# Kernel tuning notes

Hardware: AMD Instinct MI355X
Metric: run time of the kernel (lower is better)

The kernel has to match this reference:

```python
import jax, jax.numpy as jnp
import numpy as np

D_STATE = 16
LOW_RANK = 6


def _scan_fwd(t):
    # 'interwave' scan: (B, stream, signal, C, H, W) -> (stream, B, C, H*W*signal)
    st, B, C = t.shape[1], t.shape[0], t.shape[3]
    t = jnp.transpose(t, (1, 0, 3, 4, 5, 2))  # stream,B,C,H,W,signal
    return t.reshape(st, B, C, -1)


def _scan_bwd(t, sg, H, W):
    # inverse 'interwave': (stream, B, C, H*W*sg) -> (B, stream, sg, C, H, W)
    st, B, C, _ = t.shape
    t = t.reshape(st, B, C, H, W, sg)
    return jnp.transpose(t, (1, 0, 5, 2, 3, 4))


def _layernorm(t, w, b):
    # LayerNorm over last (channel) axis, eps=1e-5 (torch default)
    mu = t.mean(-1, keepdims=True)
    var = t.var(-1, keepdims=True)
    return (t - mu) * jax.lax.rsqrt(var + 1e-5) * w + b


def reference(x, x_proj_weight, dt_projs_weight, dt_projs_bias, A_logs, Ds, norm_weight, norm_bias):
    B, S, C, H, W = x.shape
    stream = S + 1
    G = 4 * stream            # scan_direction * stream groups
    N = D_STATE
    R = LOW_RANK
    L = S * H * W             # unistream_length
    i = jnp.arange(S - 1)
    j = jnp.arange(S)

    # ---- CommDiffSS2DScan (cross-scan) ----
    x_comm_0 = _scan_fwd(x[:, None])                                  # (1,B,C,L)
    x_comm_1 = _scan_fwd(jnp.swapaxes(x, -1, -2)[:, None])
    x_dif = x[:, :, None] - x[:, None, :]                             # (B,S,S,C,H,W)
    x_dif = x_dif.at[:, i, i].set(x_dif[:, i, S - 1])
    x_dif = x_dif.at[:, :, S - 1].set(x)
    x_diff_0 = _scan_fwd(x_dif)                                       # (S,B,C,L)
    x_diff_1 = _scan_fwd(jnp.swapaxes(x_dif, -1, -2))
    xs0 = jnp.concatenate([x_diff_0, x_comm_0], 0)                    # (stream,B,C,L)
    xs1 = jnp.concatenate([x_diff_1, x_comm_1], 0)
    xs = jnp.stack([xs0, xs1, xs0[..., ::-1], xs1[..., ::-1]], 0)     # (4,stream,B,C,L)
    xs = jnp.transpose(xs, (2, 0, 1, 3, 4))                           # (B,4,stream,C,L)

    # ---- input-dependent projections ----
    x_dbl = jnp.einsum('bkscl,kspc->bkspl', xs, x_proj_weight)        # (B,4,stream,R+2N,L)
    dts, Bs, Cs = jnp.split(x_dbl, [R, R + N], axis=3)
    dts = jnp.einsum('bksrl,kscr->bkscl', dts, dt_projs_weight)       # (B,4,stream,C,L)

    u = xs.reshape(B, G, C, L)
    delta = jax.nn.softplus(dts.reshape(B, G, C, L) + dt_projs_bias.reshape(G, C)[None, :, :, None])
    A = -jnp.exp(A_logs).reshape(G, C, N)
    Bm = Bs.reshape(B, G, N, L)
    Cm = Cs.reshape(B, G, N, L)

    # ---- selective scan along L ----
    def step(h, inp):
        u_, d_, b_, c_ = inp                                          # (B,G,C),(B,G,C),(B,G,N),(B,G,N)
        h = h * jnp.exp(d_[..., None] * A) + (d_ * u_)[..., None] * b_[:, :, None, :]
        return h, jnp.einsum('bgcn,bgn->bgc', h, c_)

    h0 = jnp.zeros((B, G, C, N), x.dtype)
    _, ys = jax.lax.scan(step, h0, (jnp.moveaxis(u, -1, 0), jnp.moveaxis(delta, -1, 0),
                                    jnp.moveaxis(Bm, -1, 0), jnp.moveaxis(Cm, -1, 0)))
    ys = jnp.moveaxis(ys, 0, -1) + Ds.reshape(G, C)[None, :, :, None] * u  # (B,G,C,L)

    # ---- CommDiffSS2DMerge (cross-merge) ----
    ys = jnp.transpose(ys.reshape(B, 4, stream, C, L), (1, 2, 0, 3, 4))   # (4,stream,B,C,L)
    ys = ys[:2] + ys[2:, ..., ::-1]                                       # (2,stream,B,C,L)
    yd = _scan_bwd(ys[0, :S], S, H, W) + jnp.swapaxes(_scan_bwd(ys[1, :S], S, W, H), -1, -2)
    y = yd[:, :, S - 1]
    yd = yd.at[:, i, S - 1].set(yd[:, i, i])
    yd = yd.at[:, j, j].set(0.0)
    y_dif_extend = yd.sum(2)
    y_com = (_scan_bwd(ys[0, S:], S, H, W) + jnp.swapaxes(_scan_bwd(ys[1, S:], S, W, H), -1, -2)).reshape(B, S, C, H, W)

    tocl = lambda t: jnp.transpose(t, (0, 1, 3, 4, 2))  # channels-last for out_norm
    return (_layernorm(tocl(y), norm_weight, norm_bias),
            _layernorm(tocl(y_com), norm_weight, norm_bias),
            _layernorm(tocl(y_dif_extend), norm_weight, norm_bias))


def setup_inputs() -> dict:
    key = jax.random.key(0)
    ks = jax.random.split(key, 6)
    B, S, C, H, W = 4, 2, 96, 32, 32
    stream = S + 1
    G = 4 * stream
    N, R = D_STATE, LOW_RANK
    P = N + N + R
    return {
        'x': jax.random.normal(ks[0], (B, S, C, H, W), jnp.float32),
        'x_proj_weight': jax.random.normal(ks[1], (4, stream, P, C), jnp.float32) * 0.1,
        'dt_projs_weight': jax.random.normal(ks[2], (4, stream, C, R), jnp.float32) * 0.1,
        'dt_projs_bias': jax.random.uniform(ks[3], (G * C,), jnp.float32) * 0.1,
        'A_logs': jax.random.uniform(ks[4], (G * C, N), jnp.float32),
        'Ds': jax.random.normal(ks[5], (G * C,), jnp.float32) * 0.1,
        'norm_weight': jnp.ones((C,), jnp.float32),
        'norm_bias': jnp.zeros((C,), jnp.float32),
    }
```

## Files before the change

kernel.cpp:

```cpp
#include <hip/hip_runtime.h>
#include <math.h>

typedef float f4 __attribute__((ext_vector_type(4)));
typedef float f2 __attribute__((ext_vector_type(2)));

#define L_LEN 2048
#define C_DIM 96
#define N_DIM 16
#define R_DIM 6
#define G_DIM 12
#define B_DIM 4
#define NCHUNK 64
#define CLEN 32
#define BGC (B_DIM * G_DIM * C_DIM)
#define VS 136

#define SZ_DELTA (B_DIM * G_DIM * L_LEN * C_DIM)
#define SZ_BC (B_DIM * G_DIM * N_DIM * L_LEN)
#define SZ_U6 (B_DIM * 6 * C_DIM * L_LEN)
#define SZ_Y (B_DIM * G_DIM * C_DIM * L_LEN)
#define SZ_H (BGC * NCHUNK * N_DIM)
#define SZ_S (BGC * NCHUNK)
#define SZ_X (B_DIM * 2 * C_DIM * 1024)
#define SZ_WPAD (G_DIM * 40 * C_DIM)

__device__ __forceinline__ float fexp2(float x) { return __builtin_amdgcn_exp2f(x); }
__device__ __forceinline__ f2 pkfma(f2 a, f2 b, f2 c) { return __builtin_elementwise_fma(a, b, c); }

__device__ __forceinline__ float softplus_f(float x)
{
    float sp = __logf(1.f + __expf(x));
    return (x > 20.f) ? x : sp;
}

__global__ __launch_bounds__(256) void k0_xT(
    const float* __restrict__ x, float* __restrict__ xT)
{
    __shared__ float t[32][33];
    int img = blockIdx.x;
    const float* src = x + (size_t)img * 1024;
    float* dst = xT + (size_t)img * 1024;
    int tx = threadIdx.x & 31, ty = threadIdx.x >> 5;
#pragma unroll
    for (int r = 0; r < 32; r += 8) t[ty + r][tx] = src[(ty + r) * 32 + tx];
    __syncthreads();
#pragma unroll
    for (int r = 0; r < 32; r += 8) dst[(ty + r) * 32 + tx] = t[tx][ty + r];
}

__global__ __launch_bounds__(256) void k0b_padw(
    const float* __restrict__ xpw, float* __restrict__ wpad)
{
    int i = blockIdx.x * 256 + (int)threadIdx.x;
    if (i >= G_DIM * 40 * C_DIM) return;
    int g = i / (40 * C_DIM);
    int rem = i - g * 40 * C_DIM;
    int p = rem / C_DIM, c = rem - (rem / C_DIM) * C_DIM;
    wpad[i] = (p < 38) ? xpw[((size_t)g * 38 + p) * C_DIM + c] : 0.f;
}

__global__ __launch_bounds__(256) void k1_proj(
    const float* __restrict__ x, const float* __restrict__ xT,
    const float* __restrict__ wpad, const float* __restrict__ dtw,
    const float* __restrict__ dtb,
    float* __restrict__ deltaT, float* __restrict__ Bsw,
    float* __restrict__ Csw, float* __restrict__ u6T)
{
    __shared__ char smem[C_DIM * VS * 4];
    float* Vsh = (float*)smem;
    float (*Psh)[132] = (float(*)[132])smem;

    int blk = blockIdx.x;
    int ltile = blk & 15;
    int bks = blk >> 4;
    int g = bks % G_DIM;
    int b = bks / G_DIM;
    const bool rev = (g >= 6);
    int gu = rev ? (g - 6) : g;
    int k = gu / 3, s = gu % 3;
    int l0 = ltile * 128;
    int bg = b * G_DIM + g;
    int tid = (int)threadIdx.x;

    const float* xb = (k ? xT : x) + (size_t)b * 2 * C_DIM * 1024;

#pragma unroll
    for (int j = 0; j < 12; ++j) {
        int e = tid + j * 256;
        int c = e >> 5;
        int llq = (e & 31) * 4;
        int pp = rev ? (1022 - ((l0 + llq) >> 1)) : ((l0 + llq) >> 1);
        f2 x0 = *(const f2*)(xb + (size_t)c * 1024 + pp);
        f2 x1 = *(const f2*)(xb + (size_t)(C_DIM + c) * 1024 + pp);
        f4 v;
        if (!rev) {
            if (s == 2)      { v[0] = x0.x; v[1] = x1.x; v[2] = x0.y; v[3] = x1.y; }
            else if (s == 1) { v[0] = x1.x - x0.x; v[1] = x1.x; v[2] = x1.y - x0.y; v[3] = x1.y; }
            else             { v[0] = x0.x - x1.x; v[1] = x0.x; v[2] = x0.y - x1.y; v[3] = x0.y; }
        } else {
            if (s == 2)      { v[0] = x1.y; v[1] = x0.y; v[2] = x1.x; v[3] = x0.x; }
            else if (s == 1) { v[0] = x1.y; v[1] = x1.y - x0.y; v[2] = x1.x; v[3] = x1.x - x0.x; }
            else             { v[0] = x0.y; v[1] = x0.y - x1.y; v[2] = x0.x; v[3] = x0.x - x1.x; }
        }
        *(f4*)(Vsh + c * VS + llq) = v;
    }
    __syncthreads();

    if (!rev) {
        size_t ub = ((size_t)(b * 6 + g) * L_LEN + l0) * C_DIM;
#pragma unroll
        for (int j = 0; j < 12; ++j) {
            int e = tid + j * 256;
            int lidx = e / 24;
            int c4 = (e - lidx * 24) * 4;
            f4 v = { Vsh[(c4 + 0) * VS + lidx], Vsh[(c4 + 1) * VS + lidx],
                     Vsh[(c4 + 2) * VS + lidx], Vsh[(c4 + 3) * VS + lidx] };
            *(f4*)(u6T + ub + (size_t)lidx * C_DIM + c4) = v;
        }
    }

    int ll = tid & 63;
    int P0 = __builtin_amdgcn_readfirstlane((tid >> 6) * 10);
    const float* wp = wpad + (size_t)g * 3840 + (size_t)P0 * C_DIM;

    f2 acc2[10];
#pragma unroll
    for (int p = 0; p < 10; ++p) acc2[p] = (f2){0.f, 0.f};

    for (int cb = 0; cb < C_DIM; cb += 8) {
        f2 vc2[8];
#pragma unroll
        for (int i = 0; i < 8; ++i)
            vc2[i] = *(const f2*)(Vsh + (cb + i) * VS + 2 * ll);
#pragma unroll
        for (int p = 0; p < 10; ++p) {
#pragma unroll
            for (int q = 0; q < 2; ++q) {
                f4 w = *(const f4*)(wp + p * C_DIM + cb + q * 4);
#pragma unroll
                for (int i = 0; i < 4; ++i)
                    acc2[p] = pkfma((f2){w[i], w[i]}, vc2[q * 4 + i], acc2[p]);
            }
        }
    }

    __syncthreads();
#pragma unroll
    for (int p = 0; p < 10; ++p) {
        Psh[P0 + p][2 * ll] = acc2[p].x;
        Psh[P0 + p][2 * ll + 1] = acc2[p].y;
    }
    __syncthreads();
#pragma unroll
    for (int half = 0; half < 2; ++half) {
        int q = tid & 3, lx = (tid >> 2) + half * 64;
        f4 bv = { Psh[6 + q * 4 + 0][lx], Psh[6 + q * 4 + 1][lx],
                  Psh[6 + q * 4 + 2][lx], Psh[6 + q * 4 + 3][lx] };
        *(f4*)(Bsw + ((size_t)bg * L_LEN + l0 + lx) * N_DIM + q * 4) = bv;
        f4 cv = { Psh[22 + q * 4 + 0][lx], Psh[22 + q * 4 + 1][lx],
                  Psh[22 + q * 4 + 2][lx], Psh[22 + q * 4 + 3][lx] };
        *(f4*)(Csw + ((size_t)bg * L_LEN + l0 + lx) * N_DIM + q * 4) = cv;
    }
    const float* wdg = dtw + (size_t)g * C_DIM * R_DIM;
    const float* biasg = dtb + g * C_DIM;
    size_t db = ((size_t)bg * L_LEN + l0) * C_DIM;
#pragma unroll
    for (int it = 0; it < 24; ++it) {
        int e = tid + it * 256;
        int lp = e / 96, c = e - (e / 96) * 96;
        const float* wrow = wdg + c * R_DIM;
        f2 ds2 = { biasg[c], biasg[c] };
#pragma unroll
        for (int r = 0; r < R_DIM; ++r) {
            f2 pv = { Psh[r][2 * lp], Psh[r][2 * lp + 1] };
            ds2 = pkfma((f2){wrow[r], wrow[r]}, pv, ds2);
        }
        deltaT[db + (size_t)(2 * lp) * C_DIM + c] = softplus_f(ds2.x);
        deltaT[db + (size_t)(2 * lp + 1) * C_DIM + c] = softplus_f(ds2.y);
    }
}

__global__ __launch_bounds__(192) void k2_scanA(
    const float* __restrict__ deltaT, const float* __restrict__ Bsw,
    const float* __restrict__ u6T, const float* __restrict__ A_logs,
    float* __restrict__ hend, float* __restrict__ Sbuf)
{
    __shared__ f4 Bsh[256];
    int blk = blockIdx.x;
    int chgrp = blk & 31;
    int bg = blk >> 5;
    int g = bg % G_DIM;
    int b = bg / G_DIM;
    int tid = (int)threadIdx.x;

    const f4* Bg = (const f4*)(Bsw + ((size_t)bg * L_LEN + chgrp * 64) * N_DIM);
    for (int i = tid; i < 256; i += 192) Bsh[i] = Bg[i];
    __syncthreads();

    int chl = tid / 96;
    int c = tid % 96;
    int ch = chgrp * 2 + chl;
    int bgc = bg * C_DIM + c;
    const bool rev = (g >= 6);
    int gu = rev ? (g - 6) : g;

    float a2[N_DIM];
    {
        const f4* Ap = (const f4*)(A_logs + ((size_t)g * C_DIM + c) * N_DIM);
        f4 Av[4] = { Ap[0], Ap[1], Ap[2], Ap[3] };
#pragma unroll
        for (int n = 0; n < N_DIM; ++n)
            a2[n] = -__expf(Av[n >> 2][n & 3]) * 1.44269504f;
    }

    const int LOFF = ch * CLEN;
    const float* dp = deltaT + ((size_t)bg * L_LEN + LOFF) * C_DIM + c;
    const float* up;
    int us;
    if (rev) { up = u6T + ((size_t)(b * 6 + gu) * L_LEN + (2047 - LOFF)) * C_DIM + c; us = -C_DIM; }
    else     { up = u6T + ((size_t)(b * 6 + gu) * L_LEN + LOFF) * C_DIM + c; us = C_DIM; }

    float h[N_DIM];
#pragma unroll
    for (int n = 0; n < N_DIM; ++n) h[n] = 0.f;
    float S = 0.f;

    float dbuf[4], ubuf[4];
#pragma unroll
    for (int j = 0; j < 4; ++j) { dbuf[j] = dp[j * C_DIM]; ubuf[j] = up[j * us]; }

    for (int jj = 0; jj < CLEN; jj += 4) {
        int nx = (jj + 4 < CLEN) ? jj + 4 : jj;
        float dn[4], un[4];
#pragma unroll
        for (int j = 0; j < 4; ++j) { dn[j] = dp[(nx + j) * C_DIM]; un[j] = up[(nx + j) * us]; }
#pragma unroll
        for (int j = 0; j < 4; ++j) {
            int li = chl * CLEN + jj + j;
            float d = dbuf[j];
            S += d;
            float du = d * ubuf[j];
            const f4* Bl = Bsh + (size_t)li * 4;
            f4 Bv[4] = { Bl[0], Bl[1], Bl[2], Bl[3] };
#pragma unroll
            for (int n = 0; n < N_DIM; ++n) {
                float e = fexp2(d * a2[n]);
                h[n] = fmaf(h[n], e, du * Bv[n >> 2][n & 3]);
            }
        }
#pragma unroll
        for (int j = 0; j < 4; ++j) { dbuf[j] = dn[j]; ubuf[j] = un[j]; }
    }
    float* hp = hend + ((size_t)bgc * NCHUNK + ch) * N_DIM;
#pragma unroll
    for (int q = 0; q < 4; ++q) {
        f4 hv = { h[q * 4], h[q * 4 + 1], h[q * 4 + 2], h[q * 4 + 3] };
        *(f4*)(hp + q * 4) = hv;
    }
    Sbuf[(size_t)bgc * NCHUNK + ch] = S;
}

__global__ __launch_bounds__(256) void k2_fix(
    const float* __restrict__ Sbuf, const float* __restrict__ A_logs, float* hh)
{
    int t = blockIdx.x * 256 + (int)threadIdx.x;
    int n = t & 15;
    int bgc = t >> 4;
    int c = bgc % C_DIM;
    int g = (bgc / C_DIM) % G_DIM;
    float a2 = -__expf(A_logs[((size_t)g * C_DIM + c) * N_DIM + n]) * 1.44269504f;
    const float* Sp = Sbuf + (size_t)bgc * NCHUNK;
    float h = 0.f;
    for (int ch = 0; ch < NCHUNK; ++ch) {
        size_t idx = ((size_t)bgc * NCHUNK + ch) * N_DIM + n;
        float he = hh[idx];
        float P = fexp2(a2 * Sp[ch]);
        hh[idx] = h;
        h = fmaf(h, P, he);
    }
}

__global__ __launch_bounds__(192) void k2_scanC(
    const float* __restrict__ deltaT, const float* __restrict__ Bsw,
    const float* __restrict__ Csw, const float* __restrict__ u6T,
    const float* __restrict__ A_logs, const float* __restrict__ Ds,
    const float* __restrict__ hstart, float* __restrict__ yssT)
{
    __shared__ f4 Bsh[256];
    __shared__ f4 Csh[256];
    int blk = blockIdx.x;
    int chgrp = blk & 31;
    int bg = blk >> 5;
    int g = bg % G_DIM;
    int b = bg / G_DIM;
    int tid = (int)threadIdx.x;

    const f4* Bg = (const f4*)(Bsw + ((size_t)bg * L_LEN + chgrp * 64) * N_DIM);
    const f4* Cg = (const f4*)(Csw + ((size_t)bg * L_LEN + chgrp * 64) * N_DIM);
    for (int i = tid; i < 256; i += 192) { Bsh[i] = Bg[i]; Csh[i] = Cg[i]; }
    __syncthreads();

    int chl = tid / 96;
    int c = tid % 96;
    int ch = chgrp * 2 + chl;
    int bgc = bg * C_DIM + c;
    const bool rev = (g >= 6);
    int gu = rev ? (g - 6) : g;

    float a2[N_DIM];
    {
        const f4* Ap = (const f4*)(A_logs + ((size_t)g * C_DIM + c) * N_DIM);
        f4 Av[4] = { Ap[0], Ap[1], Ap[2], Ap[3] };
#pragma unroll
        for (int n = 0; n < N_DIM; ++n)
            a2[n] = -__expf(Av[n >> 2][n & 3]) * 1.44269504f;
    }
    float dsc = Ds[g * C_DIM + c];

    const int LOFF = ch * CLEN;
    const float* dp = deltaT + ((size_t)bg * L_LEN + LOFF) * C_DIM + c;
    const float* up;
    int us;
    if (rev) { up = u6T + ((size_t)(b * 6 + gu) * L_LEN + (2047 - LOFF)) * C_DIM + c; us = -C_DIM; }
    else     { up = u6T + ((size_t)(b * 6 + gu) * L_LEN + LOFF) * C_DIM + c; us = C_DIM; }
    float* yp = yssT + ((size_t)bg * L_LEN + LOFF) * C_DIM + c;

    float h[N_DIM];
    {
        const f4* Hp = (const f4*)(hstart + ((size_t)bgc * NCHUNK + ch) * N_DIM);
        f4 Hv[4] = { Hp[0], Hp[1], Hp[2], Hp[3] };
#pragma unroll
        for (int n = 0; n < N_DIM; ++n) h[n] = Hv[n >> 2][n & 3];
    }

    float dbuf[4], ubuf[4];
#pragma unroll
    for (int j = 0; j < 4; ++j) { dbuf[j] = dp[j * C_DIM]; ubuf[j] = up[j * us]; }

    for (int jj = 0; jj < CLEN; jj += 4) {
        int nx = (jj + 4 < CLEN) ? jj + 4 : jj;
        float dn[4], un[4];
#pragma unroll
        for (int j = 0; j < 4; ++j) { dn[j] = dp[(nx + j) * C_DIM]; un[j] = up[(nx + j) * us]; }
#pragma unroll
        for (int j = 0; j < 4; ++j) {
            int li = chl * CLEN + jj + j;
            float d = dbuf[j];
            float uu = ubuf[j];
            float du = d * uu;
            const f4* Bl = Bsh + (size_t)li * 4;
            const f4* Cl = Csh + (size_t)li * 4;
            f4 Bv[4] = { Bl[0], Bl[1], Bl[2], Bl[3] };
            f4 Cv[4] = { Cl[0], Cl[1], Cl[2], Cl[3] };
            float y0 = dsc * uu, y1 = 0.f, y2 = 0.f, y3 = 0.f;
#pragma unroll
            for (int q = 0; q < 4; ++q) {
                float e0 = fexp2(d * a2[q * 4 + 0]);
                float e1 = fexp2(d * a2[q * 4 + 1]);
                float e2 = fexp2(d * a2[q * 4 + 2]);
                float e3 = fexp2(d * a2[q * 4 + 3]);
                h[q * 4 + 0] = fmaf(h[q * 4 + 0], e0, du * Bv[q][0]);
                h[q * 4 + 1] = fmaf(h[q * 4 + 1], e1, du * Bv[q][1]);
                h[q * 4 + 2] = fmaf(h[q * 4 + 2], e2, du * Bv[q][2]);
                h[q * 4 + 3] = fmaf(h[q * 4 + 3], e3, du * Bv[q][3]);
                y0 = fmaf(h[q * 4 + 0], Cv[q][0], y0);
                y1 = fmaf(h[q * 4 + 1], Cv[q][1], y1);
                y2 = fmaf(h[q * 4 + 2], Cv[q][2], y2);
                y3 = fmaf(h[q * 4 + 3], Cv[q][3], y3);
            }
            yp[(jj + j) * C_DIM] = (y0 + y1) + (y2 + y3);
        }
#pragma unroll
        for (int j = 0; j < 4; ++j) { dbuf[j] = dn[j]; ubuf[j] = un[j]; }
    }
}

__global__ __launch_bounds__(256) void k3_out(
    const float* __restrict__ yssT, const float* __restrict__ nw,
    const float* __restrict__ nb, float* __restrict__ out)
{
    __shared__ float tA[32][97];
    __shared__ float tB[32][97];
    __shared__ float ps[4][8][32];
    __shared__ float stat[4][32];

    int blk = blockIdx.x;
    int h = blk & 31;
    int bs = blk >> 5;
    int so = bs & 1;
    int b = bs >> 1;
    int tid = (int)threadIdx.x;

    auto Y = [&](int g) { return yssT + (size_t)(b * 12 + g) * L_LEN * C_DIM; };
    const float* Y0 = Y(so);
    const float* Y0r = Y(6 + so);
    const float* Y1 = Y(3 + so);
    const float* Y1r = Y(9 + so);

#pragma unroll 2
    for (int it = 0; it < 24; ++it) {
        int idx = tid + it * 256;
        int c = idx % 96, rest = idx / 96;
        int w = rest >> 1, par = rest & 1;
        int a0 = h * 64 + rest;
        int a1 = w * 64 + 2 * h + par;
        float v = Y0[(size_t)a0 * C_DIM + c] + Y0r[(size_t)(2047 - a0) * C_DIM + c]
                + Y1[(size_t)a1 * C_DIM + c] + Y1r[(size_t)(2047 - a1) * C_DIM + c];
        if (par) tA[w][c] = v; else tB[w][c] = v;
    }
    __syncthreads();

    int w = tid & 31, cg = tid >> 5;
    float sA = 0, qA = 0, sB = 0, qB = 0;
#pragma unroll
    for (int j = 0; j < 12; ++j) {
        float yv = tA[w][cg * 12 + j], dv = tB[w][cg * 12 + j];
        sA += yv; qA += yv * yv; sB += dv; qB += dv * dv;
    }
    ps[0][cg][w] = sA; ps[1][cg][w] = qA; ps[2][cg][w] = sB; ps[3][cg][w] = qB;
    __syncthreads();
    if (tid < 32) {
        int ww = tid;
        float t0 = 0, t1 = 0, t2 = 0, t3 = 0;
#pragma unroll
        for (int q = 0; q < 8; ++q) {
            t0 += ps[0][q][ww]; t1 += ps[1][q][ww];
            t2 += ps[2][q][ww]; t3 += ps[3][q][ww];
        }
        float muA = t0 * (1.f / 96.f), eqA = t1 * (1.f / 96.f);
        float muB = t2 * (1.f / 96.f), eqB = t3 * (1.f / 96.f);
        stat[0][ww] = muA; stat[1][ww] = rsqrtf(eqA - muA * muA + 1e-5f);
        stat[2][ww] = muB; stat[3][ww] = rsqrtf(eqB - muB * muB + 1e-5f);
    }
    __syncthreads();
    size_t obase = (size_t)blk * 3072;
    for (int e = tid; e < 3072; e += 256) {
        int ww = e / 96, c = e % 96;
        float wc = nw[c], bc = nb[c];
        out[obase + e] = (tA[ww][c] - stat[0][ww]) * stat[1][ww] * wc + bc;
        out[2 * 786432 + obase + e] = (tB[ww][c] - stat[2][ww]) * stat[3][ww] * wc + bc;
    }
    __syncthreads();

    const float* Y2 = Y(2);
    const float* Y2r = Y(8);
    const float* Y3 = Y(5);
    const float* Y3r = Y(11);
#pragma unroll 2
    for (int it = 0; it < 12; ++it) {
        int idx = tid + it * 256;
        int c = idx % 96, w2 = idx / 96;
        int a0 = h * 64 + 2 * w2 + so;
        int a1 = w2 * 64 + 2 * h + so;
        float v = Y2[(size_t)a0 * C_DIM + c] + Y2r[(size_t)(2047 - a0) * C_DIM + c]
                + Y3[(size_t)a1 * C_DIM + c] + Y3r[(size_t)(2047 - a1) * C_DIM + c];
        tA[w2][c] = v;
    }
    __syncthreads();
    float sC = 0, qC = 0;
#pragma unroll
    for (int j = 0; j < 12; ++j) {
        float v = tA[w][cg * 12 + j];
        sC += v; qC += v * v;
    }
    ps[0][cg][w] = sC; ps[1][cg][w] = qC;
    __syncthreads();
    if (tid < 32) {
        int ww = tid;
        float t0 = 0, t1 = 0;
#pragma unroll
        for (int q = 0; q < 8; ++q) { t0 += ps[0][q][ww]; t1 += ps[1][q][ww]; }
        float mu = t0 * (1.f / 96.f), eq = t1 * (1.f / 96.f);
        stat[0][ww] = mu; stat[1][ww] = rsqrtf(eq - mu * mu + 1e-5f);
    }
    __syncthreads();
    for (int e = tid; e < 3072; e += 256) {
        int ww = e / 96, c = e % 96;
        out[786432 + obase + e] = (tA[ww][c] - stat[0][ww]) * stat[1][ww] * nw[c] + nb[c];
    }
}

extern "C" void kernel_launch(void* const* d_in, const int* in_sizes, int n_in,
                              void* d_out, int out_size, void* d_ws, size_t ws_size,
                              hipStream_t stream)
{
    const float* x = (const float*)d_in[0];
    const float* xpw = (const float*)d_in[1];
    const float* dtw = (const float*)d_in[2];
    const float* dtb = (const float*)d_in[3];
    const float* A_logs = (const float*)d_in[4];
    const float* Ds = (const float*)d_in[5];
    const float* nw = (const float*)d_in[6];
    const float* nb = (const float*)d_in[7];
    float* out = (float*)d_out;

    float* ws = (float*)d_ws;
    float* deltaT = ws;
    float* Bsw = deltaT + SZ_DELTA;
    float* Csw = Bsw + SZ_BC;
    float* u6T = Csw + SZ_BC;
    float* yssT = u6T + SZ_U6;
    float* xT = yssT;
    float* wpad = yssT + SZ_X;
    float* hend = yssT + SZ_Y;
    float* Sbuf = hend + SZ_H;

    k0_xT<<<dim3(768), dim3(256), 0, stream>>>(x, xT);
    k0b_padw<<<dim3(180), dim3(256), 0, stream>>>(xpw, wpad);
    k1_proj<<<dim3(48 * 16), dim3(256), 0, stream>>>(x, xT, wpad, dtw, dtb, deltaT, Bsw, Csw, u6T);
    k2_scanA<<<dim3(48 * 32), dim3(192), 0, stream>>>(deltaT, Bsw, u6T, A_logs, hend, Sbuf);
    k2_fix<<<dim3(288), dim3(256), 0, stream>>>(Sbuf, A_logs, hend);
    k2_scanC<<<dim3(48 * 32), dim3(192), 0, stream>>>(deltaT, Bsw, Csw, u6T, A_logs, Ds, hend, yssT);
    k3_out<<<dim3(256), dim3(256), 0, stream>>>(yssT, nw, nb, out);
}
```

Measured before the change: 128.4 us.

## Halve scan chunk length and process two channels per thread with packed FP32 math

Scan chunk length drops from 32 to 16, so there are 128 chunks per sequence. Each thread now handles two adjacent channels with packed f2 FMAs and 8-byte loads and stores, and each block covers four chunk slots. This aims to use packed FP32 instructions and wider memory accesses while shortening the serial recurrence per thread. In exchange, the chunk-fix pass has twice as many chunks to walk serially, more hend and Sbuf traffic, and higher register pressure from the paired state.

```diff
diff --git a/kernel.cpp b/kernel.cpp
--- a/kernel.cpp
+++ b/kernel.cpp
@@ -10,8 +10,8 @@
 #define R_DIM 6
 #define G_DIM 12
 #define B_DIM 4
-#define NCHUNK 64
-#define CLEN 32
+#define NCHUNK 128
+#define CLEN 16
 #define BGC (B_DIM * G_DIM * C_DIM)
 #define VS 136
 
@@ -197,67 +197,81 @@
     for (int i = tid; i < 256; i += 192) Bsh[i] = Bg[i];
     __syncthreads();
 
-    int chl = tid / 96;
-    int c = tid % 96;
-    int ch = chgrp * 2 + chl;
-    int bgc = bg * C_DIM + c;
+    int slot = tid / 48;
+    int cp = tid % 48;
+    int c0 = cp * 2;
+    int ch = chgrp * 4 + slot;
     const bool rev = (g >= 6);
     int gu = rev ? (g - 6) : g;
 
-    float a2[N_DIM];
+    f2 a2[N_DIM];
     {
-        const f4* Ap = (const f4*)(A_logs + ((size_t)g * C_DIM + c) * N_DIM);
-        f4 Av[4] = { Ap[0], Ap[1], Ap[2], Ap[3] };
-#pragma unroll
-        for (int n = 0; n < N_DIM; ++n)
-            a2[n] = -__expf(Av[n >> 2][n & 3]) * 1.44269504f;
+        const f4* A0 = (const f4*)(A_logs + ((size_t)g * C_DIM + c0) * N_DIM);
+        const f4* A1 = (const f4*)(A_logs + ((size_t)g * C_DIM + c0 + 1) * N_DIM);
+#pragma unroll
+        for (int q = 0; q < 4; ++q) {
+            f4 v0 = A0[q], v1 = A1[q];
+#pragma unroll
+            for (int i = 0; i < 4; ++i)
+                a2[q * 4 + i] = (f2){ -__expf(v0[i]) * 1.44269504f, -__expf(v1[i]) * 1.44269504f };
+        }
     }
 
     const int LOFF = ch * CLEN;
-    const float* dp = deltaT + ((size_t)bg * L_LEN + LOFF) * C_DIM + c;
+    const int lo = slot * CLEN;
+    const float* dp = deltaT + ((size_t)bg * L_LEN + LOFF) * C_DIM + c0;
     const float* up;
     int us;
-    if (rev) { up = u6T + ((size_t)(b * 6 + gu) * L_LEN + (2047 - LOFF)) * C_DIM + c; us = -C_DIM; }
-    else     { up = u6T + ((size_t)(b * 6 + gu) * L_LEN + LOFF) * C_DIM + c; us = C_DIM; }
-
-    float h[N_DIM];
-#pragma unroll
-    for (int n = 0; n < N_DIM; ++n) h[n] = 0.f;
-    float S = 0.f;
-
-    float dbuf[4], ubuf[4];
-#pragma unroll
-    for (int j = 0; j < 4; ++j) { dbuf[j] = dp[j * C_DIM]; ubuf[j] = up[j * us]; }
+    if (rev) { up = u6T + ((size_t)(b * 6 + gu) * L_LEN + (2047 - LOFF)) * C_DIM + c0; us = -C_DIM; }
+    else     { up = u6T + ((size_t)(b * 6 + gu) * L_LEN + LOFF) * C_DIM + c0; us = C_DIM; }
+
+    f2 h2[N_DIM];
+#pragma unroll
+    for (int n = 0; n < N_DIM; ++n) h2[n] = (f2){0.f, 0.f};
+    f2 S2 = {0.f, 0.f};
+
+    f2 dbuf[4], ubuf[4];
+#pragma unroll
+    for (int j = 0; j < 4; ++j) { dbuf[j] = *(const f2*)(dp + j * C_DIM); ubuf[j] = *(const f2*)(up + j * us); }
 
     for (int jj = 0; jj < CLEN; jj += 4) {
         int nx = (jj + 4 < CLEN) ? jj + 4 : jj;
-        float dn[4], un[4];
-#pragma unroll
-        for (int j = 0; j < 4; ++j) { dn[j] = dp[(nx + j) * C_DIM]; un[j] = up[(nx + j) * us]; }
+        f2 dn[4], un[4];
+#pragma unroll
+        for (int j = 0; j < 4; ++j) { dn[j] = *(const f2*)(dp + (nx + j) * C_DIM); un[j] = *(const f2*)(up + (nx + j) * us); }
 #pragma unroll
         for (int j = 0; j < 4; ++j) {
-            int li = chl * CLEN + jj + j;
-            float d = dbuf[j];
-            S += d;
-            float du = d * ubuf[j];
+            int li = lo + jj + j;
+            f2 d2 = dbuf[j];
+            S2 += d2;
+            f2 du2 = d2 * ubuf[j];
             const f4* Bl = Bsh + (size_t)li * 4;
-            f4 Bv[4] = { Bl[0], Bl[1], Bl[2], Bl[3] };
-#pragma unroll
-            for (int n = 0; n < N_DIM; ++n) {
-                float e = fexp2(d * a2[n]);
-                h[n] = fmaf(h[n], e, du * Bv[n >> 2][n & 3]);
+#pragma unroll
+            for (int q = 0; q < 4; ++q) {
+                f4 Bq = Bl[q];
+#pragma unroll
+                for (int i = 0; i < 4; ++i) {
+                    int n = q * 4 + i;
+                    f2 m = d2 * a2[n];
+                    f2 e = { fexp2(m.x), fexp2(m.y) };
+                    h2[n] = pkfma(h2[n], e, du2 * (f2){Bq[i], Bq[i]});
+                }
             }
         }
 #pragma unroll
         for (int j = 0; j < 4; ++j) { dbuf[j] = dn[j]; ubuf[j] = un[j]; }
     }
-    float* hp = hend + ((size_t)bgc * NCHUNK + ch) * N_DIM;
+    size_t base0 = ((size_t)(bg * C_DIM + c0) * NCHUNK + ch) * N_DIM;
+    size_t base1 = base0 + (size_t)NCHUNK * N_DIM;
 #pragma unroll
     for (int q = 0; q < 4; ++q) {
-        f4 hv = { h[q * 4], h[q * 4 + 1], h[q * 4 + 2], h[q * 4 + 3] };
-        *(f4*)(hp + q * 4) = hv;
-    }
-    Sbuf[(size_t)bgc * NCHUNK + ch] = S;
+        f4 h0 = { h2[q * 4].x, h2[q * 4 + 1].x, h2[q * 4 + 2].x, h2[q * 4 + 3].x };
+        f4 h1 = { h2[q * 4].y, h2[q * 4 + 1].y, h2[q * 4 + 2].y, h2[q * 4 + 3].y };
+        *(f4*)(hend + base0 + q * 4) = h0;
+        *(f4*)(hend + base1 + q * 4) = h1;
+    }
+    Sbuf[(size_t)(bg * C_DIM + c0) * NCHUNK + ch] = S2.x;
+    Sbuf[(size_t)(bg * C_DIM + c0 + 1) * NCHUNK + ch] = S2.y;
 }
 
 __global__ __launch_bounds__(256) void k2_fix(
@@ -300,75 +314,98 @@
     for (int i = tid; i < 256; i += 192) { Bsh[i] = Bg[i]; Csh[i] = Cg[i]; }
     __syncthreads();
 
-    int chl = tid / 96;
-    int c = tid % 96;
-    int ch = chgrp * 2 + chl;
-    int bgc = bg * C_DIM + c;
+    int slot = tid / 48;
+    int cp = tid % 48;
+    int c0 = cp * 2;
+    int ch = chgrp * 4 + slot;
     const bool rev = (g >= 6);
     int gu = rev ? (g - 6) : g;
 
-    float a2[N_DIM];
+    f2 a2[N_DIM];
     {
-        const f4* Ap = (const f4*)(A_logs + ((size_t)g * C_DIM + c) * N_DIM);
-        f4 Av[4] = { Ap[0], Ap[1], Ap[2], Ap[3] };
-#pragma unroll
-        for (int n = 0; n < N_DIM; ++n)
-            a2[n] = -__expf(Av[n >> 2][n & 3]) * 1.44269504f;
-    }
-    float dsc = Ds[g * C_DIM + c];
+        const f4* A0 = (const f4*)(A_logs + ((size_t)g * C_DIM + c0) * N_DIM);
+        const f4* A1 = (const f4*)(A_logs + ((size_t)g * C_DIM + c0 + 1) * N_DIM);
+#pragma unroll
+        for (int q = 0; q < 4; ++q) {
+            f4 v0 = A0[q], v1 = A1[q];
+#pragma unroll
+            for (int i = 0; i < 4; ++i)
+                a2[q * 4 + i] = (f2){ -__expf(v0[i]) * 1.44269504f, -__expf(v1[i]) * 1.44269504f };
+        }
+    }
+    f2 dsc = *(const f2*)(Ds + g * C_DIM + c0);
 
     const int LOFF = ch * CLEN;
-    const float* dp = deltaT + ((size_t)bg * L_LEN + LOFF) * C_DIM + c;
+    const int lo = slot * CLEN;
+    const float* dp = deltaT + ((size_t)bg * L_LEN + LOFF) * C_DIM + c0;
     const float* up;
     int us;
-    if (rev) { up = u6T + ((size_t)(b * 6 + gu) * L_LEN + (2047 - LOFF)) * C_DIM + c; us = -C_DIM; }
-    else     { up = u6T + ((size_t)(b * 6 + gu) * L_LEN + LOFF) * C_DIM + c; us = C_DIM; }
-    float* yp = yssT + ((size_t)bg * L_LEN + LOFF) * C_DIM + c;
-
-    float h[N_DIM];
+    if (rev) { up = u6T + ((size_t)(b * 6 + gu) * L_LEN + (2047 - LOFF)) * C_DIM + c0; us = -C_DIM; }
+    else     { up = u6T + ((size_t)(b * 6 + gu) * L_LEN + LOFF) * C_DIM + c0; us = C_DIM; }
+    float* yp = yssT + ((size_t)bg * L_LEN + LOFF) * C_DIM + c0;
+
+    f2 h2[N_DIM];
     {
-        const f4* Hp = (const f4*)(hstart + ((size_t)bgc * NCHUNK + ch) * N_DIM);
-        f4 Hv[4] = { Hp[0], Hp[1], Hp[2], Hp[3] };
-#pragma unroll
-        for (int n = 0; n < N_DIM; ++n) h[n] = Hv[n >> 2][n & 3];
-    }
-
-    float dbuf[4], ubuf[4];
-#pragma unroll
-    for (int j = 0; j < 4; ++j) { dbuf[j] = dp[j * C_DIM]; ubuf[j] = up[j * us]; }
+        size_t base0 = ((size_t)(bg * C_DIM + c0) * NCHUNK + ch) * N_DIM;
+        size_t base1 = base0 + (size_t)NCHUNK * N_DIM;
+#pragma unroll
+        for (int q = 0; q < 4; ++q) {
+            f4 h0 = *(const f4*)(hstart + base0 + q * 4);
+            f4 h1 = *(const f4*)(hstart + base1 + q * 4);
+#pragma unroll
+            for (int i = 0; i < 4; ++i) h2[q * 4 + i] = (f2){ h0[i], h1[i] };
+        }
+    }
+
+    f2 dbuf[4], ubuf[4];
+#pragma unroll
+    for (int j = 0; j < 4; ++j) { dbuf[j] = *(const f2*)(dp + j * C_DIM); ubuf[j] = *(const f2*)(up + j * us); }
 
     for (int jj = 0; jj < CLEN; jj += 4) {
         int nx = (jj + 4 < CLEN) ? jj + 4 : jj;
-        float dn[4], un[4];
-#pragma unroll
-        for (int j = 0; j < 4; ++j) { dn[j] = dp[(nx + j) * C_DIM]; un[j] = up[(nx + j) * us]; }
+        f2 dn[4], un[4];
+#pragma unroll
+        for (int j = 0; j < 4; ++j) { dn[j] = *(const f2*)(dp + (nx + j) * C_DIM); un[j] = *(const f2*)(up + (nx + j) * us); }
 #pragma unroll
         for (int j = 0; j < 4; ++j) {
-            int li = chl * CLEN + jj + j;
-            float d = dbuf[j];
-            float uu = ubuf[j];
-            float du = d * uu;
+            int li = lo + jj + j;
+            f2 d2 = dbuf[j];
+            f2 u2 = ubuf[j];
+            f2 du2 = d2 * u2;
             const f4* Bl = Bsh + (size_t)li * 4;
             const f4* Cl = Csh + (size_t)li * 4;
-            f4 Bv[4] = { Bl[0], Bl[1], Bl[2], Bl[3] };
-            f4 Cv[4] = { Cl[0], Cl[1], Cl[2], Cl[3] };
-            float y0 = dsc * uu, y1 = 0.f, y2 = 0.f, y3 = 0.f;
+            f2 ya = dsc * u2, yb = {0.f, 0.f}, yc = {0.f, 0.f}, yd = {0.f, 0.f};
 #pragma unroll
             for (int q = 0; q < 4; ++q) {
-                float e0 = fexp2(d * a2[q * 4 + 0]);
-                float e1 = fexp2(d * a2[q * 4 + 1]);
-                float e2 = fexp2(d * a2[q * 4 + 2]);
-                float e3 = fexp2(d * a2[q * 4 + 3]);
-                h[q * 4 + 0] = fmaf(h[q * 4 + 0], e0, du * Bv[q][0]);
-                h[q * 4 + 1] = fmaf(h[q * 4 + 1], e1, du * Bv[q][1]);
-                h[q * 4 + 2] = fmaf(h[q * 4 + 2], e2, du * Bv[q][2]);
-                h[q * 4 + 3] = fmaf(h[q * 4 + 3], e3, du * Bv[q][3]);
-                y0 = fmaf(h[q * 4 + 0], Cv[q][0], y0);
-                y1 = fmaf(h[q * 4 + 1], Cv[q][1], y1);
-                y2 = fmaf(h[q * 4 + 2], Cv[q][2], y2);
-                y3 = fmaf(h[q * 4 + 3], Cv[q][3], y3);
+                f4 Bq = Bl[q];
+                f4 Cq = Cl[q];
+                {
+                    f2 m = d2 * a2[q * 4 + 0];
+                    f2 e = { fexp2(m.x), fexp2(m.y) };
+                    h2[q * 4 + 0] = pkfma(h2[q * 4 + 0], e, du2 * (f2){Bq[0], Bq[0]});
+                    ya = pkfma(h2[q * 4 + 0], (f2){Cq[0], Cq[0]}, ya);
+                }
+                {
+                    f2 m = d2 * a2[q * 4 + 1];
+                    f2 e = { fexp2(m.x), fexp2(m.y) };
+                    h2[q * 4 + 1] = pkfma(h2[q * 4 + 1], e, du2 * (f2){Bq[1], Bq[1]});
+                    yb = pkfma(h2[q * 4 + 1], (f2){Cq[1], Cq[1]}, yb);
+                }
+                {
+                    f2 m = d2 * a2[q * 4 + 2];
+                    f2 e = { fexp2(m.x), fexp2(m.y) };
+                    h2[q * 4 + 2] = pkfma(h2[q * 4 + 2], e, du2 * (f2){Bq[2], Bq[2]});
+                    yc = pkfma(h2[q * 4 + 2], (f2){Cq[2], Cq[2]}, yc);
+                }
+                {
+                    f2 m = d2 * a2[q * 4 + 3];
+                    f2 e = { fexp2(m.x), fexp2(m.y) };
+                    h2[q * 4 + 3] = pkfma(h2[q * 4 + 3], e, du2 * (f2){Bq[3], Bq[3]});
+                    yd = pkfma(h2[q * 4 + 3], (f2){Cq[3], Cq[3]}, yd);
+                }
             }
-            yp[(jj + j) * C_DIM] = (y0 + y1) + (y2 + y3);
+            f2 yv = (ya + yb) + (yc + yd);
+            *(f2*)(yp + (jj + j) * C_DIM) = yv;
         }
 #pragma unroll
         for (int j = 0; j < 4; ++j) { dbuf[j] = dn[j]; ubuf[j] = un[j]; }
```

Result: slower. 144.1 us (+12.2%).
